# Kernel tuning notes

Hardware: AMD Instinct MI355X
Metric: run time of the kernel (lower is better)

Reference implementation:

```python
import jax, jax.numpy as jnp
import numpy as np

# TT decomposition config (from Eff_TTEmbedding args in source)
P = (216, 216, 216)      # auto-factorized p_shapes for n=10,000,000 (216^3 >= n)
Q = (2, 4, 2)            # tt_q_shapes, prod = 16 = embedding_dim
R = (128, 128)           # tt_ranks
NUM_TABLES = 2
BATCH = 1024
NUM_EMB = 10_000_000


def setup_inputs() -> dict:
    key = jax.random.key(0)
    k0, k1, k2, k3 = jax.random.split(key, 4)
    # sparse indices per TT table: [n_tables, batch]
    lS_i = jax.random.randint(k3, (NUM_TABLES, BATCH), 0, NUM_EMB, dtype=jnp.int64)
    # TT cores, weight_dist='uniform'
    core0 = jax.random.uniform(k0, (NUM_TABLES, P[0], Q[0] * R[0]), dtype=jnp.float32, minval=-0.01, maxval=0.01)
    core1 = jax.random.uniform(k1, (NUM_TABLES, P[1], R[0] * Q[1] * R[1]), dtype=jnp.float32, minval=-0.01, maxval=0.01)
    core2 = jax.random.uniform(k2, (NUM_TABLES, P[2], R[1] * Q[2]), dtype=jnp.float32, minval=-0.01, maxval=0.01)
    return {"lS_i": lS_i, "core0": core0, "core1": core1, "core2": core2}


def _tt_lookup(idx, c0, c1, c2):
    """TT embedding lookup for one table. idx: [B] int; returns [B, prod(Q)]."""
    B = idx.shape[0]
    # mixed-radix decomposition of flat index into (i0, i1, i2)
    i0 = idx // (P[1] * P[2])
    i1 = (idx // P[2]) % P[1]
    i2 = idx % P[2]
    # gather TT core slices (the memory-bound irregular access)
    A = c0[i0].reshape(B, Q[0], R[0])            # [B, 2, 128]
    Bm = c1[i1].reshape(B, R[0], Q[1] * R[1])    # [B, 128, 512]
    C = c2[i2].reshape(B, R[1], Q[2])            # [B, 128, 2]
    # chained small matmuls along TT ranks
    AB = jnp.einsum('bqr,brs->bqs', A, Bm).reshape(B, Q[0] * Q[1], R[1])  # [B, 8, 128]
    out = jnp.einsum('bqr,brs->bqs', AB, C)      # [B, 8, 2]
    return out.reshape(B, Q[0] * Q[1] * Q[2])    # [B, 16]


def reference(lS_i, core0, core1, core2):
    # per-table dispatch (forward returns one embedding bag per TT table)
    return jax.vmap(_tt_lookup)(lS_i, core0, core1, core2)  # [n_tables, B, 16]
```

## Files before the change

kernel.cpp:

```cpp
#include <hip/hip_runtime.h>


#define CAP 48

__global__ __launch_bounds__(128) void tt_fused(
    const int* __restrict__ idx32,
    const float* __restrict__ c0,
    const float* __restrict__ c1,
    const float* __restrict__ c2,
    float* __restrict__ out)
{
    const int g     = blockIdx.x;
    const int q     = blockIdx.y;
    const int cs    = blockIdx.z;
    const int table = g / 216;
    const int i1    = g - table * 216;

    const int tid = threadIdx.x;
    const int rh  = tid >> 6;
    const int tl  = tid & 63;

    __shared__ float lds[2048];
    __shared__ int s_id[CAP];
    __shared__ int s_aux[CAP];
    __shared__ int s_cnt;

    if (tid < CAP) s_aux[tid] = 0;

    const bool is64 = (idx32[1] == 0) & (idx32[3] == 0) &
                      (idx32[5] == 0) & (idx32[7] == 0);

    if (rh == 0) {
        int cnt = 0;
#pragma unroll 4
        for (int it = 0; it < 16; ++it) {
            const int j  = it * 64 + tl;
            const int id = (table << 10) + j;
            const unsigned idx = is64 ? (unsigned)((const long long*)idx32)[id]
                                      : (unsigned)idx32[id];
            const unsigned i0  = idx / 46656u;
            const unsigned rem = idx - i0 * 46656u;
            const unsigned bi1 = rem / 216u;
            const bool match = ((int)bi1 == i1);
            const unsigned long long mask = __ballot(match);
            if (match) {
                const int pos = cnt + __popcll(mask & ((1ull << tl) - 1ull));
                if (pos < CAP) {
                    const unsigned i2 = rem - bi1 * 216u;
                    s_id[pos]  = id;
                    s_aux[pos] = (int)((i0 << 16) | i2);
                }
            }
            cnt += (int)__popcll(mask);
        }
        if (tl == 0) s_cnt = cnt;
    }
    __syncthreads();
    const int m = min(s_cnt, CAP);
    if (m <= cs * 8) return;

    float2*       lds2 = (float2*)lds;
    const float4* lds4 = (const float4*)lds;

    const float2* b2 = (const float2*)(c1 + ((size_t)g << 16))
                       + (size_t)rh * 64 * 256 + (q * 64 + tl);
    const float* c0t = c0 + (size_t)table * 216 * 256;

    for (int base = cs * 8; base < m; base += 16) {
        const int cl = min(8, m - base);
        __syncthreads();

#pragma unroll
        for (int l = 0; l < 8; ++l) {
            const float* ar = c0t + (size_t)(s_aux[base + l] >> 16) * 256;
#pragma unroll
            for (int k = 0; k < 2; ++k) {
                const int e = tid + 128 * k;
                lds[l * 256 + 2 * (e & 127) + (e >> 7)] = ar[e];
            }
        }
        __syncthreads();

        float2 acc[8][2];
#pragma unroll
        for (int l = 0; l < 8; ++l) {
            acc[l][0] = make_float2(0.f, 0.f);
            acc[l][1] = make_float2(0.f, 0.f);
        }

#pragma unroll 8
        for (int rr2 = 0; rr2 < 32; ++rr2) {
            const float2 bv0 = b2[(size_t)(2 * rr2) * 256];
            const float2 bv1 = b2[(size_t)(2 * rr2 + 1) * 256];
            const int rhalf = rh * 32 + rr2;
#pragma unroll
            for (int l = 0; l < 8; ++l) {
                const float4 av = lds4[l * 64 + rhalf];
                acc[l][0].x += av.x * bv0.x; acc[l][0].y += av.x * bv0.y;
                acc[l][1].x += av.y * bv0.x; acc[l][1].y += av.y * bv0.y;
                acc[l][0].x += av.z * bv1.x; acc[l][0].y += av.z * bv1.y;
                acc[l][1].x += av.w * bv1.x; acc[l][1].y += av.w * bv1.y;
            }
        }

        __syncthreads();
        if (rh == 1) {
#pragma unroll
            for (int l = 0; l < 8; ++l) {
                lds2[(l * 2 + 0) * 64 + tl] = acc[l][0];
                lds2[(l * 2 + 1) * 64 + tl] = acc[l][1];
            }
        }
        __syncthreads();

        if (rh == 0) {
#pragma unroll
            for (int l = 0; l < 8; ++l) {
                const float2 t0 = lds2[(l * 2 + 0) * 64 + tl];
                const float2 t1 = lds2[(l * 2 + 1) * 64 + tl];
                const float a0x = acc[l][0].x + t0.x, a0y = acc[l][0].y + t0.y;
                const float a1x = acc[l][1].x + t1.x, a1y = acc[l][1].y + t1.y;
                if (l < cl) {
                    const float* crow =
                        c2 + (size_t)(table * 216 + (s_aux[base + l] & 0xffff)) * 256;
                    const float4 cv = *(const float4*)(crow + 4 * tl);
                    float p00 = a0x * cv.x + a0y * cv.z;
                    float p01 = a0x * cv.y + a0y * cv.w;
                    float p10 = a1x * cv.x + a1y * cv.z;
                    float p11 = a1x * cv.y + a1y * cv.w;
#pragma unroll
                    for (int mm = 32; mm >= 1; mm >>= 1) {
                        p00 += __shfl_xor(p00, mm);
                        p01 += __shfl_xor(p01, mm);
                        p10 += __shfl_xor(p10, mm);
                        p11 += __shfl_xor(p11, mm);
                    }
                    if (tl == 0) {
                        float* o = out + (size_t)s_id[base + l] * 16;
                        *(float2*)(o + q * 2)     = make_float2(p00, p01);
                        *(float2*)(o + 8 + q * 2) = make_float2(p10, p11);
                    }
                }
            }
        }
    }
}

extern "C" void kernel_launch(void* const* d_in, const int* in_sizes, int n_in,
                              void* d_out, int out_size, void* d_ws, size_t ws_size,
                              hipStream_t stream) {
    const int*   idx = (const int*)d_in[0];
    const float* c0  = (const float*)d_in[1];
    const float* c1  = (const float*)d_in[2];
    const float* c2  = (const float*)d_in[3];
    float* out = (float*)d_out;
    (void)d_ws; (void)ws_size; (void)in_sizes; (void)n_in; (void)out_size;

    tt_fused<<<dim3(432, 4, 2), dim3(128), 0, stream>>>(idx, c0, c1, c2, out);
}
```

Baseline: 191.3 us.

## Software-pipeline core1 loads with double-buffered register batches

Replaces the rolled rank loop with four explicit batches of 16 core1 float2 loads, double-buffered in registers so the next batch's global loads are issued before the current batch's FMAs. Core0 rows are loaded into registers first and the first core1 batch is issued before the LDS store, overlapping latency with the barrier. Also fully unrolls the index-scan loop, pads the shared id arrays, and sets launch bounds to target 4 blocks per CU. The cost is much higher register pressure from 64 extra buffered floats, which could cause spills or lower occupancy.

```diff
diff --git a/kernel.cpp b/kernel.cpp
--- a/kernel.cpp
+++ b/kernel.cpp
@@ -1,9 +1,10 @@
 #include <hip/hip_runtime.h>
 
 
-#define CAP 48
+#define CAP  48
+#define CAPP (CAP + 8)
 
-__global__ __launch_bounds__(128) void tt_fused(
+__global__ __launch_bounds__(128, 4) void tt_fused(
     const int* __restrict__ idx32,
     const float* __restrict__ c0,
     const float* __restrict__ c1,
@@ -21,18 +22,18 @@
     const int tl  = tid & 63;
 
     __shared__ float lds[2048];
-    __shared__ int s_id[CAP];
-    __shared__ int s_aux[CAP];
+    __shared__ int s_id[CAPP];
+    __shared__ int s_aux[CAPP];
     __shared__ int s_cnt;
 
-    if (tid < CAP) s_aux[tid] = 0;
+    if (tid < CAPP) s_aux[tid] = 0;
 
     const bool is64 = (idx32[1] == 0) & (idx32[3] == 0) &
                       (idx32[5] == 0) & (idx32[7] == 0);
 
     if (rh == 0) {
         int cnt = 0;
-#pragma unroll 4
+#pragma unroll
         for (int it = 0; it < 16; ++it) {
             const int j  = it * 64 + tl;
             const int id = (table << 10) + j;
@@ -66,19 +67,45 @@
                        + (size_t)rh * 64 * 256 + (q * 64 + tl);
     const float* c0t = c0 + (size_t)table * 216 * 256;
 
+#define LOAD_BATCH(BUF, B)                                                  \
+    _Pragma("unroll")                                                       \
+    for (int i = 0; i < 16; ++i) BUF[i] = b2[(size_t)((B) * 16 + i) * 256];
+
+#define FMA_BATCH(BUF, B)                                                   \
+    _Pragma("unroll")                                                       \
+    for (int i2 = 0; i2 < 8; ++i2) {                                        \
+        const float2 bv0 = BUF[2 * i2];                                     \
+        const float2 bv1 = BUF[2 * i2 + 1];                                 \
+        const int rhalf = rh * 32 + (B) * 8 + i2;                           \
+        _Pragma("unroll")                                                   \
+        for (int l = 0; l < 8; ++l) {                                       \
+            const float4 av = lds4[l * 64 + rhalf];                         \
+                          \
+            acc[l][0].x += av.x * bv0.x; acc[l][0].y += av.x * bv0.y;       \
+            acc[l][1].x += av.y * bv0.x; acc[l][1].y += av.y * bv0.y;       \
+            acc[l][0].x += av.z * bv1.x; acc[l][0].y += av.z * bv1.y;       \
+            acc[l][1].x += av.w * bv1.x; acc[l][1].y += av.w * bv1.y;       \
+        }                                                                   \
+    }
+
     for (int base = cs * 8; base < m; base += 16) {
         const int cl = min(8, m - base);
         __syncthreads();
 
+        float a0[8], a1[8];
 #pragma unroll
         for (int l = 0; l < 8; ++l) {
             const float* ar = c0t + (size_t)(s_aux[base + l] >> 16) * 256;
+            a0[l] = ar[tid];
+            a1[l] = ar[tid + 128];
+        }
+
+        float2 bva[16], bvb[16];
+        LOAD_BATCH(bva, 0)
+
 #pragma unroll
-            for (int k = 0; k < 2; ++k) {
-                const int e = tid + 128 * k;
-                lds[l * 256 + 2 * (e & 127) + (e >> 7)] = ar[e];
-            }
-        }
+        for (int l = 0; l < 8; ++l)
+            lds2[l * 128 + tid] = make_float2(a0[l], a1[l]);
         __syncthreads();
 
         float2 acc[8][2];
@@ -88,20 +115,13 @@
             acc[l][1] = make_float2(0.f, 0.f);
         }
 
-#pragma unroll 8
-        for (int rr2 = 0; rr2 < 32; ++rr2) {
-            const float2 bv0 = b2[(size_t)(2 * rr2) * 256];
-            const float2 bv1 = b2[(size_t)(2 * rr2 + 1) * 256];
-            const int rhalf = rh * 32 + rr2;
-#pragma unroll
-            for (int l = 0; l < 8; ++l) {
-                const float4 av = lds4[l * 64 + rhalf];
-                acc[l][0].x += av.x * bv0.x; acc[l][0].y += av.x * bv0.y;
-                acc[l][1].x += av.y * bv0.x; acc[l][1].y += av.y * bv0.y;
-                acc[l][0].x += av.z * bv1.x; acc[l][0].y += av.z * bv1.y;
-                acc[l][1].x += av.w * bv1.x; acc[l][1].y += av.w * bv1.y;
-            }
-        }
+        LOAD_BATCH(bvb, 1)
+        FMA_BATCH(bva, 0)
+        LOAD_BATCH(bva, 2)
+        FMA_BATCH(bvb, 1)
+        LOAD_BATCH(bvb, 3)
+        FMA_BATCH(bva, 2)
+        FMA_BATCH(bvb, 3)
 
         __syncthreads();
         if (rh == 1) {
@@ -144,6 +164,8 @@
             }
         }
     }
+#undef LOAD_BATCH
+#undef FMA_BATCH
 }
 
 extern "C" void kernel_launch(void* const* d_in, const int* in_sizes, int n_in,
```

New measurement: 238.2 us. 24.5% more time.
